# Performance work log

Measured on AMD Instinct MI355X. Metric: run time of the kernel, lower is better.

## Reference

```python
import jax, jax.numpy as jnp
import numpy as np

N_NODES = 24
BATCH = 65536

def _build_edge_index():
    # hard-coded 24-node supply-chain DAG from the source: node i (i<22, even pair)
    # connects to nodes 2*(i//2)+2 and 2*(i//2)+3
    rows, cols = [], []
    for i in range(22):
        base = 2 * (i // 2) + 2
        rows += [i, i]
        cols += [base, base + 1]
    return jnp.asarray(np.stack([rows, cols]), dtype=jnp.int64)  # [2, 44]


def setup_inputs() -> dict:
    key = jax.random.key(0)
    ks = jax.random.split(key, 4)
    x = jax.random.normal(ks[0], (BATCH, N_NODES, 10), dtype=jnp.float32)
    W1 = jax.random.normal(ks[1], (10, 64), dtype=jnp.float32) * (1.0 / np.sqrt(10))
    b1 = jnp.zeros((64,), dtype=jnp.float32)
    W3 = jax.random.normal(ks[2], (64, 64), dtype=jnp.float32) * (1.0 / 8.0)
    b3 = jnp.zeros((64,), dtype=jnp.float32)
    W2 = jax.random.normal(ks[3], (64, 10), dtype=jnp.float32) * (1.0 / 8.0)
    b2 = jnp.zeros((10,), dtype=jnp.float32)
    edge_index = _build_edge_index()
    return {"x": x, "W1": W1, "b1": b1, "W3": W3, "b3": b3,
            "W2": W2, "b2": b2, "edge_index": edge_index}


def _gcn_norm(edge_index, n_nodes):
    # PyG gcn_norm with add_self_loops=True: deg counted at target (col) index
    src, dst = edge_index[0], edge_index[1]
    deg = jnp.ones((n_nodes,), jnp.float32).at[dst].add(1.0)  # self loop contributes 1
    dinv = jax.lax.rsqrt(deg)
    norm_e = dinv[src] * dinv[dst]        # [E] edge weights
    norm_self = dinv * dinv               # [N] self-loop weights
    return src, dst, norm_e, norm_self


def _gcn_conv(h, W, b, src, dst, norm_e, norm_self):
    # h: [B, N, Fin] -> [B, N, Fout]
    hw = h @ W                                             # [B, N, Fout]
    msg = hw[:, src, :] * norm_e[None, :, None]            # gather + scale [B, E, Fout]
    agg = jnp.zeros_like(hw).at[:, dst, :].add(msg)        # scatter-add over targets
    agg = agg + hw * norm_self[None, :, None]              # self loops
    return agg + b


def reference(x, W1, b1, W3, b3, W2, b2, edge_index):
    src, dst, norm_e, norm_self = _gcn_norm(edge_index, x.shape[1])
    h = jax.nn.relu(_gcn_conv(x, W1, b1, src, dst, norm_e, norm_self))
    h = jax.nn.relu(_gcn_conv(h, W3, b3, src, dst, norm_e, norm_self))
    msg = jax.nn.relu(_gcn_conv(h, W2, b2, src, dst, norm_e, norm_self))  # [B, N, 10]
    pool = jnp.mean(msg, axis=1)  # global_mean_pool over the 24 nodes -> [B, 10]
    return pool
```

## Files before the change

kernel.cpp:

```cpp
#include <hip/hip_runtime.h>
#include <hip/hip_bf16.h>


typedef __attribute__((ext_vector_type(8))) short bf16x8;
typedef __attribute__((ext_vector_type(4))) float f32x4;
typedef __attribute__((ext_vector_type(2))) float f32x2;

#define NBLK  1024
#define ITERS 8

__device__ __forceinline__ unsigned short f2bf(float f) {
  __hip_bfloat16 h = __float2bfloat16(f);
  return __builtin_bit_cast(unsigned short, h);
}
__device__ __forceinline__ f32x2 unpk(unsigned d) {
  f32x2 r;
  r.x = __builtin_bit_cast(float, d << 16);
  r.y = __builtin_bit_cast(float, d & 0xffff0000u);
  return r;
}
__device__ __forceinline__ unsigned pack2(f32x2 v) {
  return (unsigned)f2bf(v.x) | ((unsigned)f2bf(v.y) << 16);
}

union U16 { uint4 u; bf16x8 b; };

__device__ __forceinline__ bf16x8 pack8(const float v[8]) {
  U16 un;
  un.u.x = (unsigned)f2bf(v[0]) | ((unsigned)f2bf(v[1]) << 16);
  un.u.y = (unsigned)f2bf(v[2]) | ((unsigned)f2bf(v[3]) << 16);
  un.u.z = (unsigned)f2bf(v[4]) | ((unsigned)f2bf(v[5]) << 16);
  un.u.w = (unsigned)f2bf(v[6]) | ((unsigned)f2bf(v[7]) << 16);
  return un.b;
}

__global__ __launch_bounds__(256, 2)
void gnn_kernel(const float* __restrict__ xg,  const float* __restrict__ w1g,
                const float* __restrict__ b1g, const float* __restrict__ w3g,
                const float* __restrict__ b3g, const float* __restrict__ w2g,
                const float* __restrict__ b2g, float* __restrict__ outg) {
  __shared__ __align__(16) unsigned short hbuf_s[4][48 * 72];

  const int tid  = threadIdx.x;
  const int w    = tid >> 6;
  const int lane = tid & 63;
  const int l15  = lane & 15;
  const int g    = lane >> 4;
  unsigned short* hb = hbuf_s[w];
  float*          o3 = (float*)hbuf_s[w];
  const int wgid = blockIdx.x * 4 + w;

  bf16x8 w1f[4], w3f[4][2], w2f[2];
  {
    float v[8];
    #pragma unroll
    for (int mi = 0; mi < 4; ++mi) {
      const int c = 16 * mi + l15;
      #pragma unroll
      for (int j = 0; j < 8; ++j) { int k = 8 * g + j; v[j] = (k < 10) ? w1g[k * 64 + c] : 0.f; }
      w1f[mi] = pack8(v);
      #pragma unroll
      for (int ki = 0; ki < 2; ++ki) {
        #pragma unroll
        for (int j = 0; j < 8; ++j) { int k = 32 * ki + 8 * g + j; v[j] = w3g[k * 64 + c]; }
        w3f[mi][ki] = pack8(v);
      }
    }
    #pragma unroll
    for (int ki = 0; ki < 2; ++ki) {
      #pragma unroll
      for (int j = 0; j < 8; ++j) {
        int k = 32 * ki + 8 * g + j;
        v[j] = (l15 < 10) ? w2g[k * 10 + l15] : 0.f;
      }
      w2f[ki] = pack8(v);
    }
  }

  f32x2 b1r[2][4], b3r[2][4];
  #pragma unroll
  for (int ki = 0; ki < 2; ++ki) {
    #pragma unroll
    for (int p = 0; p < 4; ++p) {
      const int k = 32 * ki + 8 * g + 2 * p;
      b1r[ki][p].x = b1g[k]; b1r[ki][p].y = b1g[k + 1];
      b3r[ki][p].x = b3g[k]; b3r[ki][p].y = b3g[k + 1];
    }
  }
  const float b2p = b2g[lane % 10];

  int rowA[3], rowB[3], xoff[3];
  float csv[3], cabv[3];
  #pragma unroll
  for (int ni = 0; ni < 3; ++ni) {
    const int r   = 16 * ni + l15;
    const int sub = r / 24;
    const int n   = r - 24 * sub;
    csv[ni]  = (n < 2) ? 1.f : (1.f / 3.f);
    cabv[ni] = (n < 2) ? 0.f : ((n < 4) ? 0.57735026918962576f : (1.f / 3.f));
    const int sA = (n < 4) ? 0 : ((n & ~1) - 2);
    const int sB = (n < 4) ? 1 : ((n & ~1) - 1);
    rowA[ni] = 24 * sub + sA;
    rowB[ni] = 24 * sub + sB;
    xoff[ni] = sub * 240 + n * 10;
  }

  const f32x2 zero2 = {0.f, 0.f};

  auto build = [&](int ni, int ki, const f32x2(&bias)[4]) -> bf16x8 {
    const int kbase = 32 * ki + 8 * g;
    const uint4 vS = *(const uint4*)(hb + (16 * ni + l15) * 72 + kbase);
    const uint4 vA = *(const uint4*)(hb + rowA[ni] * 72 + kbase);
    const uint4 vB = *(const uint4*)(hb + rowB[ni] * 72 + kbase);
    const f32x2 cs2  = {csv[ni], csv[ni]};
    const f32x2 cab2 = {cabv[ni], cabv[ni]};
    const unsigned aS[4] = {vS.x, vS.y, vS.z, vS.w};
    const unsigned aA[4] = {vA.x, vA.y, vA.z, vA.w};
    const unsigned aB[4] = {vB.x, vB.y, vB.z, vB.w};
    unsigned d[4];
    #pragma unroll
    for (int p = 0; p < 4; ++p) {
      f32x2 S = unpk(aS[p]);
      f32x2 t = unpk(aA[p]) + unpk(aB[p]);
      f32x2 v = __builtin_elementwise_fma(S, cs2, bias[p]);
      v = __builtin_elementwise_fma(t, cab2, v);
      v = __builtin_elementwise_max(v, zero2);
      d[p] = pack2(v);
    }
    U16 un; un.u.x = d[0]; un.u.y = d[1]; un.u.z = d[2]; un.u.w = d[3];
    return un.b;
  };

  const f32x4 zf = {0.f, 0.f, 0.f, 0.f};

  for (int it = 0; it < ITERS; ++it) {
    const int s0 = wgid * (2 * ITERS) + it * 2;
    const float* xb = xg + (long)s0 * 240;

    f32x4 acc[4][3];
    #pragma unroll
    for (int ni = 0; ni < 3; ++ni) {
      float v[8] = {0.f, 0.f, 0.f, 0.f, 0.f, 0.f, 0.f, 0.f};
      const float* xr = xb + xoff[ni];
      if (g == 0) {
        float2 p0 = *(const float2*)(xr + 0);
        float2 p1 = *(const float2*)(xr + 2);
        float2 p2 = *(const float2*)(xr + 4);
        float2 p3 = *(const float2*)(xr + 6);
        v[0] = p0.x; v[1] = p0.y; v[2] = p1.x; v[3] = p1.y;
        v[4] = p2.x; v[5] = p2.y; v[6] = p3.x; v[7] = p3.y;
      } else if (g == 1) {
        float2 p4 = *(const float2*)(xr + 8);
        v[0] = p4.x; v[1] = p4.y;
      }
      bf16x8 bx = pack8(v);
      #pragma unroll
      for (int mi = 0; mi < 4; ++mi)
        acc[mi][ni] = __builtin_amdgcn_mfma_f32_16x16x32_bf16(w1f[mi], bx, zf, 0, 0, 0);
    }
    #pragma unroll
    for (int mi = 0; mi < 4; ++mi) {
      #pragma unroll
      for (int ni = 0; ni < 3; ++ni) {
        const int r = 16 * ni + l15, cb = 16 * mi + 4 * g;
        uint2 pk;
        pk.x = (unsigned)f2bf(acc[mi][ni][0]) | ((unsigned)f2bf(acc[mi][ni][1]) << 16);
        pk.y = (unsigned)f2bf(acc[mi][ni][2]) | ((unsigned)f2bf(acc[mi][ni][3]) << 16);
        *(uint2*)(hb + r * 72 + cb) = pk;
      }
    }

    #pragma unroll
    for (int ni = 0; ni < 3; ++ni) {
      bf16x8 bb0 = build(ni, 0, b1r[0]);
      bf16x8 bb1 = build(ni, 1, b1r[1]);
      #pragma unroll
      for (int mi = 0; mi < 4; ++mi) {
        f32x4 t = __builtin_amdgcn_mfma_f32_16x16x32_bf16(w3f[mi][0], bb0, zf, 0, 0, 0);
        acc[mi][ni] = __builtin_amdgcn_mfma_f32_16x16x32_bf16(w3f[mi][1], bb1, t, 0, 0, 0);
      }
    }
    #pragma unroll
    for (int mi = 0; mi < 4; ++mi) {
      #pragma unroll
      for (int ni = 0; ni < 3; ++ni) {
        const int r = 16 * ni + l15, cb = 16 * mi + 4 * g;
        uint2 pk;
        pk.x = (unsigned)f2bf(acc[mi][ni][0]) | ((unsigned)f2bf(acc[mi][ni][1]) << 16);
        pk.y = (unsigned)f2bf(acc[mi][ni][2]) | ((unsigned)f2bf(acc[mi][ni][3]) << 16);
        *(uint2*)(hb + r * 72 + cb) = pk;
      }
    }

    f32x4 acc3[3];
    #pragma unroll
    for (int ni = 0; ni < 3; ++ni) {
      bf16x8 bb0 = build(ni, 0, b3r[0]);
      bf16x8 bb1 = build(ni, 1, b3r[1]);
      f32x4 t  = __builtin_amdgcn_mfma_f32_16x16x32_bf16(w2f[0], bb0, zf, 0, 0, 0);
      acc3[ni] = __builtin_amdgcn_mfma_f32_16x16x32_bf16(w2f[1], bb1, t, 0, 0, 0);
    }
    #pragma unroll
    for (int ni = 0; ni < 3; ++ni) {
      const int r = 16 * ni + l15;
      *(f32x4*)(o3 + r * 20 + 4 * g) = acc3[ni];
    }

    {
      const int part = lane / 10;
      const int pc   = lane - 10 * part;
      #pragma unroll
      for (int sub = 0; sub < 2; ++sub) {
        float sum = 0.f;
        if (lane < 60) {
          const int rb = 24 * sub;
          #pragma unroll
          for (int dn = 0; dn < 4; ++dn) {
            const int n = 4 * part + dn;
            const float cs  = (n < 2) ? 1.f : (1.f / 3.f);
            const float cab = (n < 2) ? 0.f : ((n < 4) ? 0.57735026918962576f : (1.f / 3.f));
            const int sA = (n < 4) ? 0 : ((n & ~1) - 2);
            const int sB = (n < 4) ? 1 : ((n & ~1) - 1);
            const float vv = cs * o3[(rb + n) * 20 + pc]
                           + cab * (o3[(rb + sA) * 20 + pc] + o3[(rb + sB) * 20 + pc]);
            sum += fmaxf(vv + b2p, 0.f);
          }
        }
        float s1 = sum + __shfl_down(sum, 30);
        float t1 = __shfl_down(s1, 10);
        float t2 = __shfl_down(s1, 20);
        float tot = s1 + t1 + t2;
        if (lane < 10) outg[(long)(s0 + sub) * 10 + lane] = tot * (1.f / 24.f);
      }
    }
  }
}

extern "C" void kernel_launch(void* const* d_in, const int* in_sizes, int n_in,
                              void* d_out, int out_size, void* d_ws, size_t ws_size,
                              hipStream_t stream) {
  (void)in_sizes; (void)n_in; (void)d_ws; (void)ws_size; (void)out_size;
  const float* x  = (const float*)d_in[0];
  const float* W1 = (const float*)d_in[1];
  const float* b1 = (const float*)d_in[2];
  const float* W3 = (const float*)d_in[3];
  const float* b3 = (const float*)d_in[4];
  const float* W2 = (const float*)d_in[5];
  const float* b2 = (const float*)d_in[6];
  float* out = (float*)d_out;
  hipLaunchKernelGGL(gnn_kernel, dim3(NBLK), dim3(256), 0, stream,
                     x, W1, b1, W3, b3, W2, b2, out);
}
```

Baseline: 188.7 us.

## Interleave two sample pairs per wave iteration for instruction-level parallelism

Each wave now processes two independent 2-sample tiles per loop iteration, with separate LDS buffers, and interleaves their layer stages so the MFMA and LDS latencies of one tile can overlap with work on the other. The iteration count is halved so total work per wave stays the same. In exchange, LDS use per block doubles and register pressure roughly doubles because two accumulator sets are live, which risks spills or lower occupancy under launch_bounds(256,2).

```diff
diff --git a/kernel.cpp b/kernel.cpp
--- a/kernel.cpp
+++ b/kernel.cpp
@@ -7,7 +7,7 @@
 typedef __attribute__((ext_vector_type(2))) float f32x2;
 
 #define NBLK  1024
-#define ITERS 8
+#define ITERS 4
 
 __device__ __forceinline__ unsigned short f2bf(float f) {
   __hip_bfloat16 h = __float2bfloat16(f);
@@ -39,15 +39,15 @@
                 const float* __restrict__ b1g, const float* __restrict__ w3g,
                 const float* __restrict__ b3g, const float* __restrict__ w2g,
                 const float* __restrict__ b2g, float* __restrict__ outg) {
-  __shared__ __align__(16) unsigned short hbuf_s[4][48 * 72];
+  __shared__ __align__(16) unsigned short hbuf_s[4][2][48 * 72];
 
   const int tid  = threadIdx.x;
   const int w    = tid >> 6;
   const int lane = tid & 63;
   const int l15  = lane & 15;
   const int g    = lane >> 4;
-  unsigned short* hb = hbuf_s[w];
-  float*          o3 = (float*)hbuf_s[w];
+  unsigned short* hbA = hbuf_s[w][0];
+  unsigned short* hbB = hbuf_s[w][1];
   const int wgid = blockIdx.x * 4 + w;
 
   bf16x8 w1f[4], w3f[4][2], w2f[2];
@@ -106,8 +106,9 @@
   }
 
   const f32x2 zero2 = {0.f, 0.f};
-
-  auto build = [&](int ni, int ki, const f32x2(&bias)[4]) -> bf16x8 {
+  const f32x4 zf = {0.f, 0.f, 0.f, 0.f};
+
+  auto build = [&](const unsigned short* hb, int ni, int ki, const f32x2(&bias)[4]) -> bf16x8 {
     const int kbase = 32 * ki + 8 * g;
     const uint4 vS = *(const uint4*)(hb + (16 * ni + l15) * 72 + kbase);
     const uint4 vA = *(const uint4*)(hb + rowA[ni] * 72 + kbase);
@@ -131,13 +132,7 @@
     return un.b;
   };
 
-  const f32x4 zf = {0.f, 0.f, 0.f, 0.f};
-
-  for (int it = 0; it < ITERS; ++it) {
-    const int s0 = wgid * (2 * ITERS) + it * 2;
-    const float* xb = xg + (long)s0 * 240;
-
-    f32x4 acc[4][3];
+  auto layer1 = [&](const float* xb, f32x4 (&acc)[4][3]) {
     #pragma unroll
     for (int ni = 0; ni < 3; ++ni) {
       float v[8] = {0.f, 0.f, 0.f, 0.f, 0.f, 0.f, 0.f, 0.f};
@@ -158,6 +153,9 @@
       for (int mi = 0; mi < 4; ++mi)
         acc[mi][ni] = __builtin_amdgcn_mfma_f32_16x16x32_bf16(w1f[mi], bx, zf, 0, 0, 0);
     }
+  };
+
+  auto writeH = [&](unsigned short* hb, const f32x4 (&acc)[4][3]) {
     #pragma unroll
     for (int mi = 0; mi < 4; ++mi) {
       #pragma unroll
@@ -169,70 +167,90 @@
         *(uint2*)(hb + r * 72 + cb) = pk;
       }
     }
-
-    #pragma unroll
-    for (int ni = 0; ni < 3; ++ni) {
-      bf16x8 bb0 = build(ni, 0, b1r[0]);
-      bf16x8 bb1 = build(ni, 1, b1r[1]);
+  };
+
+  auto layer2 = [&](const unsigned short* hb, f32x4 (&acc)[4][3]) {
+    #pragma unroll
+    for (int ni = 0; ni < 3; ++ni) {
+      bf16x8 bb0 = build(hb, ni, 0, b1r[0]);
+      bf16x8 bb1 = build(hb, ni, 1, b1r[1]);
       #pragma unroll
       for (int mi = 0; mi < 4; ++mi) {
         f32x4 t = __builtin_amdgcn_mfma_f32_16x16x32_bf16(w3f[mi][0], bb0, zf, 0, 0, 0);
         acc[mi][ni] = __builtin_amdgcn_mfma_f32_16x16x32_bf16(w3f[mi][1], bb1, t, 0, 0, 0);
       }
     }
-    #pragma unroll
-    for (int mi = 0; mi < 4; ++mi) {
-      #pragma unroll
-      for (int ni = 0; ni < 3; ++ni) {
-        const int r = 16 * ni + l15, cb = 16 * mi + 4 * g;
-        uint2 pk;
-        pk.x = (unsigned)f2bf(acc[mi][ni][0]) | ((unsigned)f2bf(acc[mi][ni][1]) << 16);
-        pk.y = (unsigned)f2bf(acc[mi][ni][2]) | ((unsigned)f2bf(acc[mi][ni][3]) << 16);
-        *(uint2*)(hb + r * 72 + cb) = pk;
-      }
-    }
-
+  };
+
+  auto layer3 = [&](unsigned short* hb) {
     f32x4 acc3[3];
     #pragma unroll
     for (int ni = 0; ni < 3; ++ni) {
-      bf16x8 bb0 = build(ni, 0, b3r[0]);
-      bf16x8 bb1 = build(ni, 1, b3r[1]);
+      bf16x8 bb0 = build(hb, ni, 0, b3r[0]);
+      bf16x8 bb1 = build(hb, ni, 1, b3r[1]);
       f32x4 t  = __builtin_amdgcn_mfma_f32_16x16x32_bf16(w2f[0], bb0, zf, 0, 0, 0);
       acc3[ni] = __builtin_amdgcn_mfma_f32_16x16x32_bf16(w2f[1], bb1, t, 0, 0, 0);
     }
+    float* o3 = (float*)hb;
     #pragma unroll
     for (int ni = 0; ni < 3; ++ni) {
       const int r = 16 * ni + l15;
       *(f32x4*)(o3 + r * 20 + 4 * g) = acc3[ni];
     }
-
-    {
-      const int part = lane / 10;
-      const int pc   = lane - 10 * part;
-      #pragma unroll
-      for (int sub = 0; sub < 2; ++sub) {
-        float sum = 0.f;
-        if (lane < 60) {
-          const int rb = 24 * sub;
-          #pragma unroll
-          for (int dn = 0; dn < 4; ++dn) {
-            const int n = 4 * part + dn;
-            const float cs  = (n < 2) ? 1.f : (1.f / 3.f);
-            const float cab = (n < 2) ? 0.f : ((n < 4) ? 0.57735026918962576f : (1.f / 3.f));
-            const int sA = (n < 4) ? 0 : ((n & ~1) - 2);
-            const int sB = (n < 4) ? 1 : ((n & ~1) - 1);
-            const float vv = cs * o3[(rb + n) * 20 + pc]
-                           + cab * (o3[(rb + sA) * 20 + pc] + o3[(rb + sB) * 20 + pc]);
-            sum += fmaxf(vv + b2p, 0.f);
-          }
+  };
+
+  auto epilogue = [&](const unsigned short* hb, int s0) {
+    const float* o3 = (const float*)hb;
+    const int part = lane / 10;
+    const int pc   = lane - 10 * part;
+    #pragma unroll
+    for (int sub = 0; sub < 2; ++sub) {
+      float sum = 0.f;
+      if (lane < 60) {
+        const int rb = 24 * sub;
+        #pragma unroll
+        for (int dn = 0; dn < 4; ++dn) {
+          const int n = 4 * part + dn;
+          const float cs  = (n < 2) ? 1.f : (1.f / 3.f);
+          const float cab = (n < 2) ? 0.f : ((n < 4) ? 0.57735026918962576f : (1.f / 3.f));
+          const int sA = (n < 4) ? 0 : ((n & ~1) - 2);
+          const int sB = (n < 4) ? 1 : ((n & ~1) - 1);
+          const float vv = cs * o3[(rb + n) * 20 + pc]
+                         + cab * (o3[(rb + sA) * 20 + pc] + o3[(rb + sB) * 20 + pc]);
+          sum += fmaxf(vv + b2p, 0.f);
         }
-        float s1 = sum + __shfl_down(sum, 30);
-        float t1 = __shfl_down(s1, 10);
-        float t2 = __shfl_down(s1, 20);
-        float tot = s1 + t1 + t2;
-        if (lane < 10) outg[(long)(s0 + sub) * 10 + lane] = tot * (1.f / 24.f);
-      }
-    }
+      }
+      float s1 = sum + __shfl_down(sum, 30);
+      float t1 = __shfl_down(s1, 10);
+      float t2 = __shfl_down(s1, 20);
+      float tot = s1 + t1 + t2;
+      if (lane < 10) outg[(long)(s0 + sub) * 10 + lane] = tot * (1.f / 24.f);
+    }
+  };
+
+  for (int it = 0; it < ITERS; ++it) {
+    const int sA = wgid * 16 + it * 4;
+    const int sB = sA + 2;
+    const float* xbA = xg + (long)sA * 240;
+    const float* xbB = xg + (long)sB * 240;
+
+    f32x4 accA[4][3], accB[4][3];
+
+    layer1(xbA, accA);
+    layer1(xbB, accB);
+    writeH(hbA, accA);
+    writeH(hbB, accB);
+
+    layer2(hbA, accA);
+    layer2(hbB, accB);
+    writeH(hbA, accA);
+    writeH(hbB, accB);
+
+    layer3(hbA);
+    layer3(hbB);
+
+    epilogue(hbA, sA);
+    epilogue(hbB, sB);
   }
 }
 
```

Measured after the change: 188.5 us. Within noise of the previous version (-0.1%).

## Express graph aggregation as MFMA matmuls with a scaled adjacency matrix

Applied to the files above, without the earlier changes.

Replaces the scalar unpack/FMA gather-based neighbor aggregation with MFMA multiplies against a precomputed 48x48 block-diagonal mixing matrix (scaled by 3, with bias injected through an extra K column). Weights are prescaled by 1/3 to compensate, and the final mean-pool becomes a cross-lane shuffle reduction over the MFMA output. This moves VALU and LDS gather work onto matrix cores, at the cost of more MFMAs, extra LDS buffers and transposed layouts, plus additional bf16 rounding of intermediate values.

```diff
diff --git a/kernel.cpp b/kernel.cpp
--- a/kernel.cpp
+++ b/kernel.cpp
@@ -4,7 +4,6 @@
 
 typedef __attribute__((ext_vector_type(8))) short bf16x8;
 typedef __attribute__((ext_vector_type(4))) float f32x4;
-typedef __attribute__((ext_vector_type(2))) float f32x2;
 
 #define NBLK  1024
 #define ITERS 8
@@ -12,15 +11,6 @@
 __device__ __forceinline__ unsigned short f2bf(float f) {
   __hip_bfloat16 h = __float2bfloat16(f);
   return __builtin_bit_cast(unsigned short, h);
-}
-__device__ __forceinline__ f32x2 unpk(unsigned d) {
-  f32x2 r;
-  r.x = __builtin_bit_cast(float, d << 16);
-  r.y = __builtin_bit_cast(float, d & 0xffff0000u);
-  return r;
-}
-__device__ __forceinline__ unsigned pack2(f32x2 v) {
-  return (unsigned)f2bf(v.x) | ((unsigned)f2bf(v.y) << 16);
 }
 
 union U16 { uint4 u; bf16x8 b; };
@@ -33,115 +23,118 @@
   un.u.w = (unsigned)f2bf(v[6]) | ((unsigned)f2bf(v[7]) << 16);
   return un.b;
 }
+__device__ __forceinline__ uint2 pk4(f32x4 a) {
+  uint2 r;
+  r.x = (unsigned)f2bf(a[0]) | ((unsigned)f2bf(a[1]) << 16);
+  r.y = (unsigned)f2bf(a[2]) | ((unsigned)f2bf(a[3]) << 16);
+  return r;
+}
+__device__ __forceinline__ uint2 pk4r(f32x4 a) {
+  const f32x4 z = {0.f, 0.f, 0.f, 0.f};
+  return pk4(__builtin_elementwise_max(a, z));
+}
 
 __global__ __launch_bounds__(256, 2)
 void gnn_kernel(const float* __restrict__ xg,  const float* __restrict__ w1g,
                 const float* __restrict__ b1g, const float* __restrict__ w3g,
                 const float* __restrict__ b3g, const float* __restrict__ w2g,
                 const float* __restrict__ b2g, float* __restrict__ outg) {
-  __shared__ __align__(16) unsigned short hbuf_s[4][48 * 72];
+  __shared__ __align__(16) unsigned short bufA_s[4][64 * 72];
+  __shared__ __align__(16) unsigned short bufB_s[4][48 * 72];
+  __shared__ __align__(16) unsigned short bufD_s[4][16 * 72];
 
   const int tid  = threadIdx.x;
   const int w    = tid >> 6;
   const int lane = tid & 63;
   const int l15  = lane & 15;
   const int g    = lane >> 4;
-  unsigned short* hb = hbuf_s[w];
-  float*          o3 = (float*)hbuf_s[w];
+  unsigned short* bA = bufA_s[w];
+  unsigned short* bB = bufB_s[w];
+  unsigned short* bD = bufD_s[w];
   const int wgid = blockIdx.x * 4 + w;
 
-  bf16x8 w1f[4], w3f[4][2], w2f[2];
+  bf16x8 w1bf[4], w3f[4][2], w2f[2], amixB[3][2];
   {
     float v[8];
     #pragma unroll
-    for (int mi = 0; mi < 4; ++mi) {
-      const int c = 16 * mi + l15;
-      #pragma unroll
-      for (int j = 0; j < 8; ++j) { int k = 8 * g + j; v[j] = (k < 10) ? w1g[k * 64 + c] : 0.f; }
-      w1f[mi] = pack8(v);
-      #pragma unroll
-      for (int ki = 0; ki < 2; ++ki) {
+    for (int nc = 0; nc < 4; ++nc) {
+      #pragma unroll
+      for (int j = 0; j < 8; ++j) { int k = 8 * g + j; v[j] = (k < 10) ? w1g[k * 64 + 16 * nc + l15] : 0.f; }
+      w1bf[nc] = pack8(v);
+      #pragma unroll
+      for (int ks = 0; ks < 2; ++ks) {
         #pragma unroll
-        for (int j = 0; j < 8; ++j) { int k = 32 * ki + 8 * g + j; v[j] = w3g[k * 64 + c]; }
-        w3f[mi][ki] = pack8(v);
-      }
-    }
-    #pragma unroll
-    for (int ki = 0; ki < 2; ++ki) {
+        for (int j = 0; j < 8; ++j) v[j] = w3g[(32 * ks + 8 * g + j) * 64 + 16 * nc + l15] * (1.f / 3.f);
+        w3f[nc][ks] = pack8(v);
+      }
+    }
+    #pragma unroll
+    for (int ks = 0; ks < 2; ++ks) {
       #pragma unroll
       for (int j = 0; j < 8; ++j) {
-        int k = 32 * ki + 8 * g + j;
-        v[j] = (l15 < 10) ? w2g[k * 10 + l15] : 0.f;
-      }
-      w2f[ki] = pack8(v);
-    }
-  }
-
-  f32x2 b1r[2][4], b3r[2][4];
+        int k = 32 * ks + 8 * g + j;
+        v[j] = (l15 < 10) ? w2g[k * 10 + l15] * (1.f / 3.f) : 0.f;
+      }
+      w2f[ks] = pack8(v);
+    }
+    #pragma unroll
+    for (int nn = 0; nn < 3; ++nn) {
+      #pragma unroll
+      for (int ks = 0; ks < 2; ++ks) {
+        #pragma unroll
+        for (int j = 0; j < 8; ++j) {
+          const int k = 32 * ks + 8 * g + j, n = 16 * nn + l15;
+          float c = 0.f;
+          if (k == 48) c = 3.f;
+          else if (k < 48 && (k / 24) == (n / 24)) {
+            const int s = k % 24, t = n % 24;
+            if (t < 2)      c = (s == t) ? 3.f : 0.f;
+            else if (t < 4) c = (s == t) ? 1.f : ((s < 2) ? 1.7320508075688772f : 0.f);
+            else { const int sa = (t & ~1) - 2; c = (s == t || s == sa || s == sa + 1) ? 1.f : 0.f; }
+          }
+          v[j] = c;
+        }
+        amixB[nn][ks] = pack8(v);
+      }
+    }
+  }
+
+  const unsigned short b1f = f2bf(b1g[lane]);
+  const unsigned short b3f = f2bf(b3g[lane]);
+
+  {
+    const uint4 z4 = {0, 0, 0, 0};
+    *(uint4*)&bA[lane * 72 + 48] = z4;
+    *(uint4*)&bA[lane * 72 + 56] = z4;
+    *(uint4*)&bA[lane * 72 + 64] = z4;
+    if (lane < 16) {
+      *(uint4*)&bD[lane * 72 + 48] = z4;
+      *(uint4*)&bD[lane * 72 + 56] = z4;
+      *(uint4*)&bD[lane * 72 + 64] = z4;
+      bD[lane * 72 + 48] = (lane < 10) ? f2bf(b2g[lane]) : (unsigned short)0;
+    }
+  }
+
+  int xoff[3];
   #pragma unroll
-  for (int ki = 0; ki < 2; ++ki) {
-    #pragma unroll
-    for (int p = 0; p < 4; ++p) {
-      const int k = 32 * ki + 8 * g + 2 * p;
-      b1r[ki][p].x = b1g[k]; b1r[ki][p].y = b1g[k + 1];
-      b3r[ki][p].x = b3g[k]; b3r[ki][p].y = b3g[k + 1];
-    }
-  }
-  const float b2p = b2g[lane % 10];
-
-  int rowA[3], rowB[3], xoff[3];
-  float csv[3], cabv[3];
-  #pragma unroll
-  for (int ni = 0; ni < 3; ++ni) {
-    const int r   = 16 * ni + l15;
-    const int sub = r / 24;
-    const int n   = r - 24 * sub;
-    csv[ni]  = (n < 2) ? 1.f : (1.f / 3.f);
-    cabv[ni] = (n < 2) ? 0.f : ((n < 4) ? 0.57735026918962576f : (1.f / 3.f));
-    const int sA = (n < 4) ? 0 : ((n & ~1) - 2);
-    const int sB = (n < 4) ? 1 : ((n & ~1) - 1);
-    rowA[ni] = 24 * sub + sA;
-    rowB[ni] = 24 * sub + sB;
-    xoff[ni] = sub * 240 + n * 10;
-  }
-
-  const f32x2 zero2 = {0.f, 0.f};
-
-  auto build = [&](int ni, int ki, const f32x2(&bias)[4]) -> bf16x8 {
-    const int kbase = 32 * ki + 8 * g;
-    const uint4 vS = *(const uint4*)(hb + (16 * ni + l15) * 72 + kbase);
-    const uint4 vA = *(const uint4*)(hb + rowA[ni] * 72 + kbase);
-    const uint4 vB = *(const uint4*)(hb + rowB[ni] * 72 + kbase);
-    const f32x2 cs2  = {csv[ni], csv[ni]};
-    const f32x2 cab2 = {cabv[ni], cabv[ni]};
-    const unsigned aS[4] = {vS.x, vS.y, vS.z, vS.w};
-    const unsigned aA[4] = {vA.x, vA.y, vA.z, vA.w};
-    const unsigned aB[4] = {vB.x, vB.y, vB.z, vB.w};
-    unsigned d[4];
-    #pragma unroll
-    for (int p = 0; p < 4; ++p) {
-      f32x2 S = unpk(aS[p]);
-      f32x2 t = unpk(aA[p]) + unpk(aB[p]);
-      f32x2 v = __builtin_elementwise_fma(S, cs2, bias[p]);
-      v = __builtin_elementwise_fma(t, cab2, v);
-      v = __builtin_elementwise_max(v, zero2);
-      d[p] = pack2(v);
-    }
-    U16 un; un.u.x = d[0]; un.u.y = d[1]; un.u.z = d[2]; un.u.w = d[3];
-    return un.b;
-  };
+  for (int mt = 0; mt < 3; ++mt) {
+    const int r = 16 * mt + l15, sub = r / 24, n = r - 24 * sub;
+    xoff[mt] = sub * 240 + n * 10;
+  }
 
   const f32x4 zf = {0.f, 0.f, 0.f, 0.f};
 
   for (int it = 0; it < ITERS; ++it) {
-    const int s0 = wgid * (2 * ITERS) + it * 2;
-    const float* xb = xg + (long)s0 * 240;
-
-    f32x4 acc[4][3];
-    #pragma unroll
-    for (int ni = 0; ni < 3; ++ni) {
+    const int sp = wgid * 16 + it * 2;
+    const float* xb = xg + (long)sp * 240;
+
+    bA[lane * 72 + 48] = b1f;
+
+    f32x4 acc1[3][4];
+    #pragma unroll
+    for (int mt = 0; mt < 3; ++mt) {
       float v[8] = {0.f, 0.f, 0.f, 0.f, 0.f, 0.f, 0.f, 0.f};
-      const float* xr = xb + xoff[ni];
+      const float* xr = xb + xoff[mt];
       if (g == 0) {
         float2 p0 = *(const float2*)(xr + 0);
         float2 p1 = *(const float2*)(xr + 2);
@@ -153,84 +146,125 @@
         float2 p4 = *(const float2*)(xr + 8);
         v[0] = p4.x; v[1] = p4.y;
       }
-      bf16x8 bx = pack8(v);
-      #pragma unroll
-      for (int mi = 0; mi < 4; ++mi)
-        acc[mi][ni] = __builtin_amdgcn_mfma_f32_16x16x32_bf16(w1f[mi], bx, zf, 0, 0, 0);
-    }
-    #pragma unroll
-    for (int mi = 0; mi < 4; ++mi) {
-      #pragma unroll
-      for (int ni = 0; ni < 3; ++ni) {
-        const int r = 16 * ni + l15, cb = 16 * mi + 4 * g;
-        uint2 pk;
-        pk.x = (unsigned)f2bf(acc[mi][ni][0]) | ((unsigned)f2bf(acc[mi][ni][1]) << 16);
-        pk.y = (unsigned)f2bf(acc[mi][ni][2]) | ((unsigned)f2bf(acc[mi][ni][3]) << 16);
-        *(uint2*)(hb + r * 72 + cb) = pk;
-      }
-    }
-
-    #pragma unroll
-    for (int ni = 0; ni < 3; ++ni) {
-      bf16x8 bb0 = build(ni, 0, b1r[0]);
-      bf16x8 bb1 = build(ni, 1, b1r[1]);
-      #pragma unroll
-      for (int mi = 0; mi < 4; ++mi) {
-        f32x4 t = __builtin_amdgcn_mfma_f32_16x16x32_bf16(w3f[mi][0], bb0, zf, 0, 0, 0);
-        acc[mi][ni] = __builtin_amdgcn_mfma_f32_16x16x32_bf16(w3f[mi][1], bb1, t, 0, 0, 0);
-      }
-    }
-    #pragma unroll
-    for (int mi = 0; mi < 4; ++mi) {
-      #pragma unroll
-      for (int ni = 0; ni < 3; ++ni) {
-        const int r = 16 * ni + l15, cb = 16 * mi + 4 * g;
-        uint2 pk;
-        pk.x = (unsigned)f2bf(acc[mi][ni][0]) | ((unsigned)f2bf(acc[mi][ni][1]) << 16);
-        pk.y = (unsigned)f2bf(acc[mi][ni][2]) | ((unsigned)f2bf(acc[mi][ni][3]) << 16);
-        *(uint2*)(hb + r * 72 + cb) = pk;
-      }
-    }
-
-    f32x4 acc3[3];
-    #pragma unroll
-    for (int ni = 0; ni < 3; ++ni) {
-      bf16x8 bb0 = build(ni, 0, b3r[0]);
-      bf16x8 bb1 = build(ni, 1, b3r[1]);
-      f32x4 t  = __builtin_amdgcn_mfma_f32_16x16x32_bf16(w2f[0], bb0, zf, 0, 0, 0);
-      acc3[ni] = __builtin_amdgcn_mfma_f32_16x16x32_bf16(w2f[1], bb1, t, 0, 0, 0);
-    }
-    #pragma unroll
-    for (int ni = 0; ni < 3; ++ni) {
-      const int r = 16 * ni + l15;
-      *(f32x4*)(o3 + r * 20 + 4 * g) = acc3[ni];
+      bf16x8 ax = pack8(v);
+      #pragma unroll
+      for (int nc = 0; nc < 4; ++nc)
+        acc1[mt][nc] = __builtin_amdgcn_mfma_f32_16x16x32_bf16(ax, w1bf[nc], zf, 0, 0, 0);
+    }
+    #pragma unroll
+    for (int mt = 0; mt < 3; ++mt)
+      #pragma unroll
+      for (int nc = 0; nc < 4; ++nc)
+        *(uint2*)&bA[(16 * nc + l15) * 72 + 16 * mt + 4 * g] = pk4(acc1[mt][nc]);
+
+    U16 a2[4][2];
+    #pragma unroll
+    for (int mi = 0; mi < 4; ++mi)
+      #pragma unroll
+      for (int ks = 0; ks < 2; ++ks)
+        a2[mi][ks].u = *(const uint4*)&bA[(16 * mi + l15) * 72 + 32 * ks + 8 * g];
+    bA[lane * 72 + 48] = b3f;
+    f32x4 acc2[4][3];
+    #pragma unroll
+    for (int mi = 0; mi < 4; ++mi)
+      #pragma unroll
+      for (int nn = 0; nn < 3; ++nn) {
+        f32x4 t = __builtin_amdgcn_mfma_f32_16x16x32_bf16(a2[mi][0].b, amixB[nn][0], zf, 0, 0, 0);
+        acc2[mi][nn] = __builtin_amdgcn_mfma_f32_16x16x32_bf16(a2[mi][1].b, amixB[nn][1], t, 0, 0, 0);
+      }
+    #pragma unroll
+    for (int mi = 0; mi < 4; ++mi)
+      #pragma unroll
+      for (int nn = 0; nn < 3; ++nn)
+        *(uint2*)&bB[(16 * nn + l15) * 72 + 16 * mi + 4 * g] = pk4r(acc2[mi][nn]);
+
+    U16 a3[3][2];
+    #pragma unroll
+    for (int mt = 0; mt < 3; ++mt)
+      #pragma unroll
+      for (int ks = 0; ks < 2; ++ks)
+        a3[mt][ks].u = *(const uint4*)&bB[(16 * mt + l15) * 72 + 32 * ks + 8 * g];
+    f32x4 acc3[3][4];
+    #pragma unroll
+    for (int mt = 0; mt < 3; ++mt)
+      #pragma unroll
+      for (int nc = 0; nc < 4; ++nc) {
+        f32x4 t = __builtin_amdgcn_mfma_f32_16x16x32_bf16(a3[mt][0].b, w3f[nc][0], zf, 0, 0, 0);
+        acc3[mt][nc] = __builtin_amdgcn_mfma_f32_16x16x32_bf16(a3[mt][1].b, w3f[nc][1], t, 0, 0, 0);
+      }
+    #pragma unroll
+    for (int mt = 0; mt < 3; ++mt)
+      #pragma unroll
+      for (int nc = 0; nc < 4; ++nc)
+        *(uint2*)&bA[(16 * nc + l15) * 72 + 16 * mt + 4 * g] = pk4(acc3[mt][nc]);
+
+    U16 a4[4][2];
+    #pragma unroll
+    for (int mi = 0; mi < 4; ++mi)
+      #pragma unroll
+      for (int ks = 0; ks < 2; ++ks)
+        a4[mi][ks].u = *(const uint4*)&bA[(16 * mi + l15) * 72 + 32 * ks + 8 * g];
+    f32x4 acc4[4][3];
+    #pragma unroll
+    for (int mi = 0; mi < 4; ++mi)
+      #pragma unroll
+      for (int nn = 0; nn < 3; ++nn) {
+        f32x4 t = __builtin_amdgcn_mfma_f32_16x16x32_bf16(a4[mi][0].b, amixB[nn][0], zf, 0, 0, 0);
+        acc4[mi][nn] = __builtin_amdgcn_mfma_f32_16x16x32_bf16(a4[mi][1].b, amixB[nn][1], t, 0, 0, 0);
+      }
+    #pragma unroll
+    for (int mi = 0; mi < 4; ++mi)
+      #pragma unroll
+      for (int nn = 0; nn < 3; ++nn)
+        *(uint2*)&bB[(16 * nn + l15) * 72 + 16 * mi + 4 * g] = pk4r(acc4[mi][nn]);
+
+    U16 a5[3][2];
+    #pragma unroll
+    for (int mt = 0; mt < 3; ++mt)
+      #pragma unroll
+      for (int ks = 0; ks < 2; ++ks)
+        a5[mt][ks].u = *(const uint4*)&bB[(16 * mt + l15) * 72 + 32 * ks + 8 * g];
+    f32x4 acc5[3];
+    #pragma unroll
+    for (int mt = 0; mt < 3; ++mt) {
+      f32x4 t = __builtin_amdgcn_mfma_f32_16x16x32_bf16(a5[mt][0].b, w2f[0], zf, 0, 0, 0);
+      acc5[mt] = __builtin_amdgcn_mfma_f32_16x16x32_bf16(a5[mt][1].b, w2f[1], t, 0, 0, 0);
+    }
+    #pragma unroll
+    for (int mt = 0; mt < 3; ++mt)
+      *(uint2*)&bD[l15 * 72 + 16 * mt + 4 * g] = pk4(acc5[mt]);
+
+    U16 a6[2];
+    #pragma unroll
+    for (int ks = 0; ks < 2; ++ks)
+      a6[ks].u = *(const uint4*)&bD[l15 * 72 + 32 * ks + 8 * g];
+    f32x4 acc6[3];
+    #pragma unroll
+    for (int nt = 0; nt < 3; ++nt) {
+      f32x4 t = __builtin_amdgcn_mfma_f32_16x16x32_bf16(a6[0].b, amixB[nt][0], zf, 0, 0, 0);
+      acc6[nt] = __builtin_amdgcn_mfma_f32_16x16x32_bf16(a6[1].b, amixB[nt][1], t, 0, 0, 0);
     }
 
     {
-      const int part = lane / 10;
-      const int pc   = lane - 10 * part;
-      #pragma unroll
-      for (int sub = 0; sub < 2; ++sub) {
-        float sum = 0.f;
-        if (lane < 60) {
-          const int rb = 24 * sub;
-          #pragma unroll
-          for (int dn = 0; dn < 4; ++dn) {
-            const int n = 4 * part + dn;
-            const float cs  = (n < 2) ? 1.f : (1.f / 3.f);
-            const float cab = (n < 2) ? 0.f : ((n < 4) ? 0.57735026918962576f : (1.f / 3.f));
-            const int sA = (n < 4) ? 0 : ((n & ~1) - 2);
-            const int sB = (n < 4) ? 1 : ((n & ~1) - 1);
-            const float vv = cs * o3[(rb + n) * 20 + pc]
-                           + cab * (o3[(rb + sA) * 20 + pc] + o3[(rb + sB) * 20 + pc]);
-            sum += fmaxf(vv + b2p, 0.f);
-          }
+      f32x4 v0 = __builtin_elementwise_max(acc6[0], zf);
+      f32x4 v1 = __builtin_elementwise_max(acc6[1], zf);
+      f32x4 v2 = __builtin_elementwise_max(acc6[2], zf);
+      f32x4 sum0 = v0, sum1 = v2;
+      if (l15 < 8) sum0 += v1; else sum1 += v1;
+      #pragma unroll
+      for (int d = 1; d < 16; d <<= 1) {
+        #pragma unroll
+        for (int r = 0; r < 4; ++r) {
+          sum0[r] += __shfl_xor(sum0[r], d);
+          sum1[r] += __shfl_xor(sum1[r], d);
         }
-        float s1 = sum + __shfl_down(sum, 30);
-        float t1 = __shfl_down(s1, 10);
-        float t2 = __shfl_down(s1, 20);
-        float tot = s1 + t1 + t2;
-        if (lane < 10) outg[(long)(s0 + sub) * 10 + lane] = tot * (1.f / 24.f);
+      }
+      if (l15 < 2) {
+        const f32x4 s = (l15 == 0) ? sum0 : sum1;
+        const float sc = 1.f / 72.f;
+        const long  so = (long)(sp + l15) * 10;
+        if (g < 3) { float2 t0 = {s[0] * sc, s[1] * sc}; *(float2*)&outg[so + 4 * g] = t0; }
+        if (g < 2) { float2 t1 = {s[2] * sc, s[3] * sc}; *(float2*)&outg[so + 4 * g + 2] = t1; }
       }
     }
   }
```

After: 183.5 us. 2.7% less time.
